# Performance work log

Hardware: AMD Instinct MI355X
Metric: run time of the kernel (lower is better)

The kernel has to match this reference:

```python
import jax, jax.numpy as jnp
import numpy as np

EPS = 1e-5
N_GRAPHS = 64


def gcn_conv(x, W, b, src, dst, n_nodes):
    # GCNConv: out = D^{-1/2} (A + I) D^{-1/2} X W + b
    xw = x @ W  # [N, H]
    # add self loops
    loops = jnp.arange(n_nodes, dtype=src.dtype)
    src_f = jnp.concatenate([src, loops])
    dst_f = jnp.concatenate([dst, loops])
    deg = jax.ops.segment_sum(jnp.ones_like(dst_f, dtype=xw.dtype), dst_f, num_segments=n_nodes)
    dinv = jnp.where(deg > 0, jax.lax.rsqrt(deg), 0.0)
    norm = dinv[src_f] * dinv[dst_f]  # [E+N]
    msg = xw[src_f] * norm[:, None]  # gather + scale
    out = jax.ops.segment_sum(msg, dst_f, num_segments=n_nodes)  # scatter-add
    return out + b


def batchnorm(x):
    # fresh BatchNorm1d in training mode: identity affine, batch stats, biased var
    mean = jnp.mean(x, axis=0)
    var = jnp.mean((x - mean) ** 2, axis=0)
    return (x - mean) * jax.lax.rsqrt(var + EPS)


def setup_inputs() -> dict:
    key = jax.random.key(0)
    ks = jax.random.split(key, 12)
    N, E, F, H, C = 65536, 1048576, 64, 64, 16
    x = jax.random.normal(ks[0], (N, F), dtype=jnp.float32)
    edge_index = jax.random.randint(ks[1], (2, E), 0, N, dtype=jnp.int64)
    batch = jnp.sort(jax.random.randint(ks[2], (N,), 0, N_GRAPHS, dtype=jnp.int64))
    s = 1.0 / np.sqrt(H)
    W0 = jax.random.normal(ks[3], (F, H), dtype=jnp.float32) * s
    b0 = jax.random.normal(ks[4], (H,), dtype=jnp.float32) * 0.1
    W1 = jax.random.normal(ks[5], (H, H), dtype=jnp.float32) * s
    b1 = jax.random.normal(ks[6], (H,), dtype=jnp.float32) * 0.1
    W2 = jax.random.normal(ks[7], (H, H), dtype=jnp.float32) * s
    b2 = jax.random.normal(ks[8], (H,), dtype=jnp.float32) * 0.1
    clf_W = jax.random.normal(ks[9], (C, H), dtype=jnp.float32) * s
    clf_b = jax.random.normal(ks[10], (C,), dtype=jnp.float32) * 0.1
    return {"x": x, "edge_index": edge_index, "batch": batch,
            "W0": W0, "b0": b0, "W1": W1, "b1": b1, "W2": W2, "b2": b2,
            "clf_W": clf_W, "clf_b": clf_b}


def reference(x, edge_index, batch, W0, b0, W1, b1, W2, b2, clf_W, clf_b):
    n_nodes = x.shape[0]
    src, dst = edge_index[0], edge_index[1]
    weights = [(W0, b0), (W1, b1), (W2, b2)]
    n_conv = len(weights)
    h = x
    for i, (W, b) in enumerate(weights):
        h = gcn_conv(h, W, b, src, dst, n_nodes)
        if i < n_conv - 1:
            h = jax.nn.relu(h)
        h = batchnorm(h)
    # global mean pool over graphs
    sums = jax.ops.segment_sum(h, batch, num_segments=N_GRAPHS)
    cnts = jax.ops.segment_sum(jnp.ones((n_nodes,), h.dtype), batch, num_segments=N_GRAPHS)
    pooled = sums / jnp.maximum(cnts, 1.0)[:, None]
    logits = pooled @ clf_W.T + clf_b
    return jax.nn.softmax(logits, axis=1)
```

## Files before the change

kernel.cpp:

```cpp
#include <hip/hip_runtime.h>
#include <hip/hip_fp16.h>


#define NBKT 512
#define CAP  4096
#define BSTRIDE 16
#define NSLOT 16
#define GSL   2048

__device__ inline unsigned pack2h(float a, float b) {
    __half ha = __float2half_rn(a), hb = __float2half_rn(b);
    unsigned short ua = *(unsigned short*)&ha, ub = *(unsigned short*)&hb;
    return (unsigned)ua | ((unsigned)ub << 16);
}

__device__ inline void acc8(float* a, uint4 u) {
    __half2* hp = (__half2*)&u;
#pragma unroll
    for (int i = 0; i < 4; ++i) {
        float2 f = __half22float2(hp[i]);
        a[2 * i] += f.x;
        a[2 * i + 1] += f.y;
    }
}

__global__ void k_binit(int* __restrict__ bcur, float* __restrict__ gstats) {
    int idx = blockIdx.x * 256 + threadIdx.x;
    if (idx < NBKT) bcur[idx * BSTRIDE] = idx * CAP;
    for (int i = idx; i < 3 * NSLOT * GSL; i += 32768) gstats[i] = 0.0f;
}

__global__ void k_bin(const int* __restrict__ ei, int E, int* __restrict__ bcur,
                      int* __restrict__ buck) {
    __shared__ int sd[4096];
    __shared__ unsigned short bk[4096];
    __shared__ int cnt[NBKT], off[NBKT];
    int t = threadIdx.x;
    int base = blockIdx.x * 4096;
    for (int i = t; i < NBKT; i += 256) cnt[i] = 0;
    __syncthreads();
#pragma unroll
    for (int k = 0; k < 16; ++k) {
        int i = k * 256 + t;
        int e = base + i;
        int s = ei[e], d = ei[E + e];
        sd[i] = (s << 7) | (d & 127);
        int b = d >> 7;
        bk[i] = (unsigned short)b;
        atomicAdd(&cnt[b], 1);
    }
    __syncthreads();
    for (int b = t; b < NBKT; b += 256) {
        int c = cnt[b];
        off[b] = c ? atomicAdd(&bcur[b * BSTRIDE], c) : 0;
    }
    __syncthreads();
#pragma unroll
    for (int k = 0; k < 16; ++k) {
        int i = k * 256 + t;
        int b = bk[i];
        int p = atomicAdd(&off[b], 1);
        buck[p] = sd[i];
    }
}

__global__ __launch_bounds__(512) void k_place(
        const int* __restrict__ bcur, const int* __restrict__ buck,
        int* __restrict__ rowptr, float* __restrict__ dinv, int* __restrict__ csr,
        int N, int E) {
    __shared__ int s[NBKT];
    __shared__ int dc[128], sc[128], cur[128];
    __shared__ int sbase;
    int b = blockIdx.x, t = threadIdx.x;
    s[t] = bcur[t * BSTRIDE] - t * CAP;
    if (t < 128) dc[t] = 0;
    __syncthreads();
    for (int o = 1; o < NBKT; o <<= 1) {
        int x = (t >= o) ? s[t - o] : 0;
        __syncthreads();
        s[t] += x;
        __syncthreads();
    }
    if (t == 0) {
        sbase = (b == 0) ? 0 : s[b - 1];
        if (b == NBKT - 1) rowptr[N] = E;
    }
    __syncthreads();
    int beg = b * CAP, end = bcur[b * BSTRIDE];
    for (int i = beg + t; i < end; i += 512) atomicAdd(&dc[buck[i] & 127], 1);
    __syncthreads();
    int v = (t < 128) ? dc[t] : 0;
    if (t < 128) sc[t] = v;
    __syncthreads();
    for (int o = 1; o < 128; o <<= 1) {
        int x = 0;
        if (t < 128 && t >= o) x = sc[t - o];
        __syncthreads();
        if (t < 128) sc[t] += x;
        __syncthreads();
    }
    if (t < 128) {
        int r = sbase + sc[t] - v;
        rowptr[b * 128 + t] = r;
        cur[t] = r;
        dinv[b * 128 + t] = rsqrtf((float)(v + 1));
    }
    __syncthreads();
    for (int i = beg + t; i < end; i += 512) {
        int e = buck[i];
        int p = atomicAdd(&cur[e & 127], 1);
        csr[p] = e >> 7;
    }
}

template <int HIN, int HS>
__global__ void k_gemm(const void* __restrict__ hv, const float* __restrict__ W,
                       const float* __restrict__ gstats, float invN,
                       const float* __restrict__ dinv, __half* __restrict__ y) {
    __shared__ float Ws[4096];
    __shared__ float hs[64 * 65];
    __shared__ float sm[64], sr[64], bs[64];
    int t = threadIdx.x;
    int rowBase = blockIdx.x * 64;
    if (t < 64) {
        if (HS) {
            float S = 0.0f, Q = 0.0f;
#pragma unroll
            for (int c = 0; c < NSLOT; ++c) {
                S += gstats[c * GSL + t * 16];
                Q += gstats[c * GSL + (64 + t) * 16];
            }
            float m = S * invN;
            float var = Q * invN - m * m;
            sm[t] = m;
            sr[t] = rsqrtf(var + 1e-5f);
        } else {
            sm[t] = 0.0f;
            sr[t] = 1.0f;
        }
    }
    __syncthreads();
#pragma unroll
    for (int k = 0; k < 4; ++k) {
        int i = t + k * 256;
        float4 wv = ((const float4*)W)[i];
        float s = sr[i >> 4];
        wv.x *= s; wv.y *= s; wv.z *= s; wv.w *= s;
        ((float4*)Ws)[i] = wv;
    }
    if (HIN) {
        const uint4* src = (const uint4*)((const __half*)hv + (size_t)rowBase * 64);
#pragma unroll
        for (int k = 0; k < 2; ++k) {
            int i = t + k * 256;
            int row = i >> 3, c8 = i & 7;
            uint4 u = src[i];
            const __half2* hp = (const __half2*)&u;
            float* dst = &hs[row * 65 + c8 * 8];
#pragma unroll
            for (int j = 0; j < 4; ++j) {
                dst[2 * j + 0] = __low2float(hp[j]);
                dst[2 * j + 1] = __high2float(hp[j]);
            }
        }
    } else {
        const float4* src = (const float4*)((const float*)hv + (size_t)rowBase * 64);
#pragma unroll
        for (int k = 0; k < 4; ++k) {
            int i = t + k * 256;
            int row = i >> 4, c4 = i & 15;
            float4 v = src[i];
            float* dst = &hs[row * 65 + c4 * 4];
            dst[0] = v.x; dst[1] = v.y; dst[2] = v.z; dst[3] = v.w;
        }
    }
    __syncthreads();
    if (t < 64) {
        float acc = 0.0f;
        for (int f = 0; f < 64; ++f) acc += sm[f] * Ws[f * 64 + t];
        bs[t] = -acc;
    }
    __syncthreads();
    int rg = t >> 4;
    int cg = t & 15;
    float4 a0, a1, a2, a3;
    {
        float bx = bs[cg * 4 + 0], by = bs[cg * 4 + 1];
        float bz = bs[cg * 4 + 2], bw = bs[cg * 4 + 3];
        a0 = {bx, by, bz, bw}; a1 = a0; a2 = a0; a3 = a0;
    }
    const float* h0 = &hs[(rg * 4 + 0) * 65];
    const float* h1 = &hs[(rg * 4 + 1) * 65];
    const float* h2 = &hs[(rg * 4 + 2) * 65];
    const float* h3 = &hs[(rg * 4 + 3) * 65];
#pragma unroll 4
    for (int f = 0; f < 64; ++f) {
        float4 wv = ((float4*)Ws)[f * 16 + cg];
        float v0 = h0[f], v1 = h1[f], v2 = h2[f], v3 = h3[f];
        a0.x += v0 * wv.x; a0.y += v0 * wv.y; a0.z += v0 * wv.z; a0.w += v0 * wv.w;
        a1.x += v1 * wv.x; a1.y += v1 * wv.y; a1.z += v1 * wv.z; a1.w += v1 * wv.w;
        a2.x += v2 * wv.x; a2.y += v2 * wv.y; a2.z += v2 * wv.z; a2.w += v2 * wv.w;
        a3.x += v3 * wv.x; a3.y += v3 * wv.y; a3.z += v3 * wv.z; a3.w += v3 * wv.w;
    }
    float d0 = dinv[rowBase + rg * 4 + 0];
    float d1 = dinv[rowBase + rg * 4 + 1];
    float d2 = dinv[rowBase + rg * 4 + 2];
    float d3 = dinv[rowBase + rg * 4 + 3];
    uint2* y2 = (uint2*)y;
    size_t ob = (size_t)(rowBase + rg * 4) * 16 + cg;
    y2[ob + 0]  = {pack2h(a0.x * d0, a0.y * d0), pack2h(a0.z * d0, a0.w * d0)};
    y2[ob + 16] = {pack2h(a1.x * d1, a1.y * d1), pack2h(a1.z * d1, a1.w * d1)};
    y2[ob + 32] = {pack2h(a2.x * d2, a2.y * d2), pack2h(a2.z * d2, a2.w * d2)};
    y2[ob + 48] = {pack2h(a3.x * d3, a3.y * d3), pack2h(a3.z * d3, a3.w * d3)};
}

template <int RELU>
__global__ __launch_bounds__(512) void k_agg(
        const __half* __restrict__ y, const int* __restrict__ rowptr,
        const int* __restrict__ csr, const float* __restrict__ dinv,
        const float* __restrict__ bias, __half* __restrict__ hout,
        float* __restrict__ gstats, int N) {
    __shared__ int lcsr[2048];
    __shared__ int lrp[65];
    __shared__ float SW[16][64];
    int t = threadIdx.x;
    int lane = t & 63, wid = t >> 6;
    int o = lane >> 3, j = lane & 7;
    int nodeBase = blockIdx.x * 64;
    if (t < 65) lrp[t] = rowptr[nodeBase + t];
    __syncthreads();
    int wbase = lrp[0];
    int wlen = lrp[64] - wbase;
    bool fits = (wlen <= 2048);
    if (fits)
        for (int i = t; i < wlen; i += 512) lcsr[i] = csr[wbase + i];
    __syncthreads();

    int n = nodeBase + wid * 8 + o;
    int beg = lrp[wid * 8 + o] - wbase;
    int d = lrp[wid * 8 + o + 1] - wbase - beg;
    const uint4* y4 = (const uint4*)y;
    float a[8] = {0, 0, 0, 0, 0, 0, 0, 0};

    if (fits) {
        const int* cp = lcsr + beg;
        int k = 0;
        for (; k + 4 <= d; k += 4) {
            int s0 = cp[k], s1 = cp[k + 1], s2 = cp[k + 2], s3 = cp[k + 3];
            uint4 u0 = y4[(size_t)s0 * 8 + j];
            uint4 u1 = y4[(size_t)s1 * 8 + j];
            uint4 u2 = y4[(size_t)s2 * 8 + j];
            uint4 u3 = y4[(size_t)s3 * 8 + j];
            acc8(a, u0); acc8(a, u1); acc8(a, u2); acc8(a, u3);
        }
        for (; k < d; ++k) {
            uint4 u0 = y4[(size_t)cp[k] * 8 + j];
            acc8(a, u0);
        }
    } else {
        const int* cp = csr + wbase + beg;
        int k = 0;
        for (; k + 4 <= d; k += 4) {
            int s0 = cp[k], s1 = cp[k + 1], s2 = cp[k + 2], s3 = cp[k + 3];
            uint4 u0 = y4[(size_t)s0 * 8 + j];
            uint4 u1 = y4[(size_t)s1 * 8 + j];
            uint4 u2 = y4[(size_t)s2 * 8 + j];
            uint4 u3 = y4[(size_t)s3 * 8 + j];
            acc8(a, u0); acc8(a, u1); acc8(a, u2); acc8(a, u3);
        }
        for (; k < d; ++k) {
            uint4 u0 = y4[(size_t)cp[k] * 8 + j];
            acc8(a, u0);
        }
    }
    uint4 us = y4[(size_t)n * 8 + j];
    acc8(a, us);

    float dv = dinv[n];
    const float4* b4 = (const float4*)bias;
    float4 blo = b4[j * 2], bhi = b4[j * 2 + 1];
    float v[8];
    v[0] = a[0] * dv + blo.x; v[1] = a[1] * dv + blo.y;
    v[2] = a[2] * dv + blo.z; v[3] = a[3] * dv + blo.w;
    v[4] = a[4] * dv + bhi.x; v[5] = a[5] * dv + bhi.y;
    v[6] = a[6] * dv + bhi.z; v[7] = a[7] * dv + bhi.w;
    if (RELU) {
#pragma unroll
        for (int i = 0; i < 8; ++i) v[i] = fmaxf(v[i], 0.0f);
    }
    uint4 ov;
    ov.x = pack2h(v[0], v[1]); ov.y = pack2h(v[2], v[3]);
    ov.z = pack2h(v[4], v[5]); ov.w = pack2h(v[6], v[7]);
    ((uint4*)hout)[(size_t)n * 8 + j] = ov;

    float q[8];
#pragma unroll
    for (int i = 0; i < 8; ++i) q[i] = v[i] * v[i];
#pragma unroll
    for (int st = 8; st <= 32; st <<= 1) {
#pragma unroll
        for (int i = 0; i < 8; ++i) {
            v[i] += __shfl_xor(v[i], st);
            q[i] += __shfl_xor(q[i], st);
        }
    }
    if (o == 0) {
#pragma unroll
        for (int i = 0; i < 8; ++i) {
            SW[wid][j * 8 + i] = v[i];
            SW[8 + wid][j * 8 + i] = q[i];
        }
    }
    __syncthreads();
    if (t < 64) {
        float s = 0.0f, qq = 0.0f;
#pragma unroll
        for (int w = 0; w < 8; ++w) {
            s += SW[w][t];
            qq += SW[8 + w][t];
        }
        float* gs = gstats + (blockIdx.x & (NSLOT - 1)) * GSL;
        atomicAdd(&gs[t * 16], s);
        atomicAdd(&gs[(64 + t) * 16], qq);
    }
}

__global__ __launch_bounds__(512) void k_poolhead(
        const __half* __restrict__ h, const int* __restrict__ batch,
        const float* __restrict__ gstats, float invN,
        const float* __restrict__ clfW, const float* __restrict__ clfb,
        float* __restrict__ out, int N) {
    __shared__ float SWm[8][64];
    __shared__ float pooled[64];
    __shared__ int rng[2];
    int g = blockIdx.x;
    int t = threadIdx.x;
    int lane = t & 63, wid = t >> 6;
    int o = lane >> 3, j = lane & 7;
    if (t < 2) {
        int key = g + t, lo = 0, hi = N;
        while (lo < hi) {
            int mid = (lo + hi) >> 1;
            if (batch[mid] < key) lo = mid + 1; else hi = mid;
        }
        rng[t] = lo;
    }
    __syncthreads();
    int lo = rng[0], hi = rng[1];
    const uint4* h4 = (const uint4*)h;
    float a[8] = {0, 0, 0, 0, 0, 0, 0, 0};
    int slot = wid * 8 + o;
    for (int n = lo + slot; n < hi; n += 256) {
        int n1 = n + 64, n2 = n + 128, n3 = n + 192;
        uint4 u0 = h4[(size_t)n * 8 + j];
        uint4 u1 = h4[(size_t)min(n1, hi - 1) * 8 + j];
        uint4 u2 = h4[(size_t)min(n2, hi - 1) * 8 + j];
        uint4 u3 = h4[(size_t)min(n3, hi - 1) * 8 + j];
        acc8(a, u0);
        if (n1 < hi) acc8(a, u1);
        if (n2 < hi) acc8(a, u2);
        if (n3 < hi) acc8(a, u3);
    }
#pragma unroll
    for (int st = 8; st <= 32; st <<= 1) {
#pragma unroll
        for (int i = 0; i < 8; ++i) a[i] += __shfl_xor(a[i], st);
    }
    if (o == 0) {
#pragma unroll
        for (int i = 0; i < 8; ++i) SWm[wid][j * 8 + i] = a[i];
    }
    __syncthreads();
    if (t < 64) {
        float s = 0.0f;
#pragma unroll
        for (int w = 0; w < 8; ++w) s += SWm[w][t];
        float S = 0.0f, Q = 0.0f;
#pragma unroll
        for (int c = 0; c < NSLOT; ++c) {
            S += gstats[c * GSL + t * 16];
            Q += gstats[c * GSL + (64 + t) * 16];
        }
        float m = S * invN;
        float r = rsqrtf(Q * invN - m * m + 1e-5f);
        float mean = s / fmaxf((float)(hi - lo), 1.0f);
        pooled[t] = (mean - m) * r;
    }
    __syncthreads();
    if (t < 16) {
        float acc = 0.0f;
#pragma unroll 8
        for (int f = 0; f < 64; ++f) acc += pooled[f] * clfW[t * 64 + f];
        acc += clfb[t];
        float mx = acc;
#pragma unroll
        for (int oo = 1; oo < 16; oo <<= 1) mx = fmaxf(mx, __shfl_xor(mx, oo, 16));
        float e = __expf(acc - mx);
        float sum = e;
#pragma unroll
        for (int oo = 1; oo < 16; oo <<= 1) sum += __shfl_xor(sum, oo, 16);
        out[g * 16 + t] = e / sum;
    }
}

extern "C" void kernel_launch(void* const* d_in, const int* in_sizes, int n_in,
                              void* d_out, int out_size, void* d_ws, size_t ws_size,
                              hipStream_t stream) {
    const float* x    = (const float*)d_in[0];
    const int*   ei   = (const int*)d_in[1];
    const int*   bat  = (const int*)d_in[2];
    const float* W0   = (const float*)d_in[3];
    const float* b0   = (const float*)d_in[4];
    const float* W1   = (const float*)d_in[5];
    const float* b1   = (const float*)d_in[6];
    const float* W2   = (const float*)d_in[7];
    const float* b2   = (const float*)d_in[8];
    const float* clfW = (const float*)d_in[9];
    const float* clfb = (const float*)d_in[10];
    float* out = (float*)d_out;

    const int N = in_sizes[0] / 64;
    const int E = in_sizes[1] / 2;
    const int AB = N / 64;

    char* w = (char*)d_ws;
    size_t off = 0;
    auto take = [&](size_t bytes) -> void* {
        off = (off + 255) & ~(size_t)255;
        void* p = w + off;
        off += bytes;
        return p;
    };
    int*    rowptr   = (int*)take((size_t)(N + 1) * 4);
    int*    bcur     = (int*)take((size_t)NBKT * BSTRIDE * 4);
    float*  dinv     = (float*)take((size_t)N * 4);
    int*    csr      = (int*)take((size_t)E * 4);
    __half* y        = (__half*)take((size_t)N * 64 * 2);
    __half* hA       = (__half*)take((size_t)N * 64 * 2);
    __half* hB       = (__half*)take((size_t)N * 64 * 2);
    float*  gstats   = (float*)take((size_t)3 * NSLOT * GSL * 4);
    int* buck = (int*)hB;
    float* gs0 = gstats;
    float* gs1 = gstats + NSLOT * GSL;
    float* gs2 = gstats + 2 * NSLOT * GSL;

    const float invN = 1.0f / (float)N;

    k_binit<<<128, 256, 0, stream>>>(bcur, gstats);
    k_bin<<<E / 4096, 256, 0, stream>>>(ei, E, bcur, buck);
    k_place<<<NBKT, 512, 0, stream>>>(bcur, buck, rowptr, dinv, csr, N, E);

    k_gemm<0, 0><<<N / 64, 256, 0, stream>>>(x, W0, nullptr, invN, dinv, y);
    k_agg<1><<<AB, 512, 0, stream>>>(y, rowptr, csr, dinv, b0, hA, gs0, N);
    k_gemm<1, 1><<<N / 64, 256, 0, stream>>>(hA, W1, gs0, invN, dinv, y);
    k_agg<1><<<AB, 512, 0, stream>>>(y, rowptr, csr, dinv, b1, hB, gs1, N);
    k_gemm<1, 1><<<N / 64, 256, 0, stream>>>(hB, W2, gs1, invN, dinv, y);
    k_agg<0><<<AB, 512, 0, stream>>>(y, rowptr, csr, dinv, b2, hA, gs2, N);

    k_poolhead<<<64, 512, 0, stream>>>(hA, bat, gs2, invN, clfW, clfb, out, N);
}
```

Before: 165.7 us.

## Fuse GCN layers into a single cooperative persistent kernel with grid syncs

The three gemm/aggregate layer pairs and the pooling head are merged into one cooperative kernel of 256 blocks of 512 threads, with grid-wide syncs between phases. Each block loops over four 64-row tiles or windows, so W and the BN stats are staged once per block rather than once per 64 rows. This removes six kernel launch boundaries and the repeated per-block setup. The cost is that only 256 blocks run, which means fewer waves hiding gather latency in the aggregation, plus grid-sync overhead; a plain multi-launch fallback runs if the cooperative launch fails.

```diff
diff --git a/kernel.cpp b/kernel.cpp
--- a/kernel.cpp
+++ b/kernel.cpp
@@ -1,5 +1,8 @@
 #include <hip/hip_runtime.h>
 #include <hip/hip_fp16.h>
+#include <hip/hip_cooperative_groups.h>
+
+namespace cg = cooperative_groups;
 
 
 #define NBKT 512
@@ -7,6 +10,7 @@
 #define BSTRIDE 16
 #define NSLOT 16
 #define GSL   2048
+#define FB    256
 
 __device__ inline unsigned pack2h(float a, float b) {
     __half ha = __float2half_rn(a), hb = __float2half_rn(b);
@@ -113,15 +117,17 @@
     }
 }
 
+
 template <int HIN, int HS>
-__global__ void k_gemm(const void* __restrict__ hv, const float* __restrict__ W,
-                       const float* __restrict__ gstats, float invN,
-                       const float* __restrict__ dinv, __half* __restrict__ y) {
-    __shared__ float Ws[4096];
-    __shared__ float hs[64 * 65];
-    __shared__ float sm[64], sr[64], bs[64];
-    int t = threadIdx.x;
-    int rowBase = blockIdx.x * 64;
+__device__ void gemm_phase(const void* __restrict__ hv, const float* __restrict__ W,
+                           const float* __restrict__ gstats, float invN,
+                           const float* __restrict__ dinv, __half* __restrict__ y,
+                           float* smem, int t) {
+    float* Ws = smem;
+    float* hs = smem + 4096;
+    float* sm = smem + 8256;
+    float* sr = smem + 8320;
+    float* bs = smem + 8384;
     if (t < 64) {
         if (HS) {
             float S = 0.0f, Q = 0.0f;
@@ -131,9 +137,8 @@
                 Q += gstats[c * GSL + (64 + t) * 16];
             }
             float m = S * invN;
-            float var = Q * invN - m * m;
             sm[t] = m;
-            sr[t] = rsqrtf(var + 1e-5f);
+            sr[t] = rsqrtf(Q * invN - m * m + 1e-5f);
         } else {
             sm[t] = 0.0f;
             sr[t] = 1.0f;
@@ -141,18 +146,27 @@
     }
     __syncthreads();
 #pragma unroll
-    for (int k = 0; k < 4; ++k) {
-        int i = t + k * 256;
+    for (int k = 0; k < 2; ++k) {
+        int i = t + k * 512;
         float4 wv = ((const float4*)W)[i];
         float s = sr[i >> 4];
         wv.x *= s; wv.y *= s; wv.z *= s; wv.w *= s;
         ((float4*)Ws)[i] = wv;
     }
-    if (HIN) {
-        const uint4* src = (const uint4*)((const __half*)hv + (size_t)rowBase * 64);
-#pragma unroll
-        for (int k = 0; k < 2; ++k) {
-            int i = t + k * 256;
+    __syncthreads();
+    if (t < 64) {
+        float acc = 0.0f;
+        for (int f = 0; f < 64; ++f) acc += sm[f] * Ws[f * 64 + t];
+        bs[t] = -acc;
+    }
+    __syncthreads();
+    int rg = t >> 4;
+    int cg = t & 15;
+    for (int tile = 0; tile < 4; ++tile) {
+        int rowBase = (blockIdx.x * 4 + tile) * 64;
+        if (HIN) {
+            const uint4* src = (const uint4*)((const __half*)hv + (size_t)rowBase * 64);
+            int i = t;
             int row = i >> 3, c8 = i & 7;
             uint4 u = src[i];
             const __half2* hp = (const __half2*)&u;
@@ -162,88 +176,72 @@
                 dst[2 * j + 0] = __low2float(hp[j]);
                 dst[2 * j + 1] = __high2float(hp[j]);
             }
-        }
-    } else {
-        const float4* src = (const float4*)((const float*)hv + (size_t)rowBase * 64);
-#pragma unroll
-        for (int k = 0; k < 4; ++k) {
-            int i = t + k * 256;
-            int row = i >> 4, c4 = i & 15;
-            float4 v = src[i];
-            float* dst = &hs[row * 65 + c4 * 4];
-            dst[0] = v.x; dst[1] = v.y; dst[2] = v.z; dst[3] = v.w;
-        }
-    }
-    __syncthreads();
-    if (t < 64) {
-        float acc = 0.0f;
-        for (int f = 0; f < 64; ++f) acc += sm[f] * Ws[f * 64 + t];
-        bs[t] = -acc;
-    }
-    __syncthreads();
-    int rg = t >> 4;
-    int cg = t & 15;
-    float4 a0, a1, a2, a3;
-    {
-        float bx = bs[cg * 4 + 0], by = bs[cg * 4 + 1];
-        float bz = bs[cg * 4 + 2], bw = bs[cg * 4 + 3];
-        a0 = {bx, by, bz, bw}; a1 = a0; a2 = a0; a3 = a0;
-    }
-    const float* h0 = &hs[(rg * 4 + 0) * 65];
-    const float* h1 = &hs[(rg * 4 + 1) * 65];
-    const float* h2 = &hs[(rg * 4 + 2) * 65];
-    const float* h3 = &hs[(rg * 4 + 3) * 65];
+        } else {
+            const float4* src = (const float4*)((const float*)hv + (size_t)rowBase * 64);
+#pragma unroll
+            for (int k = 0; k < 2; ++k) {
+                int i = t + k * 512;
+                int row = i >> 4, c4 = i & 15;
+                float4 v = src[i];
+                float* dst = &hs[row * 65 + c4 * 4];
+                dst[0] = v.x; dst[1] = v.y; dst[2] = v.z; dst[3] = v.w;
+            }
+        }
+        __syncthreads();
+        float4 a0, a1;
+        {
+            float bx = bs[cg * 4 + 0], by = bs[cg * 4 + 1];
+            float bz = bs[cg * 4 + 2], bw = bs[cg * 4 + 3];
+            a0 = {bx, by, bz, bw}; a1 = a0;
+        }
+        const float* h0 = &hs[(rg * 2 + 0) * 65];
+        const float* h1 = &hs[(rg * 2 + 1) * 65];
 #pragma unroll 4
-    for (int f = 0; f < 64; ++f) {
-        float4 wv = ((float4*)Ws)[f * 16 + cg];
-        float v0 = h0[f], v1 = h1[f], v2 = h2[f], v3 = h3[f];
-        a0.x += v0 * wv.x; a0.y += v0 * wv.y; a0.z += v0 * wv.z; a0.w += v0 * wv.w;
-        a1.x += v1 * wv.x; a1.y += v1 * wv.y; a1.z += v1 * wv.z; a1.w += v1 * wv.w;
-        a2.x += v2 * wv.x; a2.y += v2 * wv.y; a2.z += v2 * wv.z; a2.w += v2 * wv.w;
-        a3.x += v3 * wv.x; a3.y += v3 * wv.y; a3.z += v3 * wv.z; a3.w += v3 * wv.w;
-    }
-    float d0 = dinv[rowBase + rg * 4 + 0];
-    float d1 = dinv[rowBase + rg * 4 + 1];
-    float d2 = dinv[rowBase + rg * 4 + 2];
-    float d3 = dinv[rowBase + rg * 4 + 3];
-    uint2* y2 = (uint2*)y;
-    size_t ob = (size_t)(rowBase + rg * 4) * 16 + cg;
-    y2[ob + 0]  = {pack2h(a0.x * d0, a0.y * d0), pack2h(a0.z * d0, a0.w * d0)};
-    y2[ob + 16] = {pack2h(a1.x * d1, a1.y * d1), pack2h(a1.z * d1, a1.w * d1)};
-    y2[ob + 32] = {pack2h(a2.x * d2, a2.y * d2), pack2h(a2.z * d2, a2.w * d2)};
-    y2[ob + 48] = {pack2h(a3.x * d3, a3.y * d3), pack2h(a3.z * d3, a3.w * d3)};
+        for (int f = 0; f < 64; ++f) {
+            float4 wv = ((float4*)Ws)[f * 16 + cg];
+            float v0 = h0[f], v1 = h1[f];
+            a0.x += v0 * wv.x; a0.y += v0 * wv.y; a0.z += v0 * wv.z; a0.w += v0 * wv.w;
+            a1.x += v1 * wv.x; a1.y += v1 * wv.y; a1.z += v1 * wv.z; a1.w += v1 * wv.w;
+        }
+        float d0 = dinv[rowBase + rg * 2 + 0];
+        float d1 = dinv[rowBase + rg * 2 + 1];
+        uint2* y2 = (uint2*)y;
+        size_t ob = (size_t)(rowBase + rg * 2) * 16 + cg;
+        y2[ob + 0]  = {pack2h(a0.x * d0, a0.y * d0), pack2h(a0.z * d0, a0.w * d0)};
+        y2[ob + 16] = {pack2h(a1.x * d1, a1.y * d1), pack2h(a1.z * d1, a1.w * d1)};
+        __syncthreads();
+    }
 }
 
 template <int RELU>
-__global__ __launch_bounds__(512) void k_agg(
-        const __half* __restrict__ y, const int* __restrict__ rowptr,
-        const int* __restrict__ csr, const float* __restrict__ dinv,
-        const float* __restrict__ bias, __half* __restrict__ hout,
-        float* __restrict__ gstats, int N) {
-    __shared__ int lcsr[2048];
-    __shared__ int lrp[65];
-    __shared__ float SW[16][64];
-    int t = threadIdx.x;
+__device__ void agg_phase(const __half* __restrict__ y, const int* __restrict__ rowptr,
+                          const int* __restrict__ csr, const float* __restrict__ dinv,
+                          const float* __restrict__ bias, __half* __restrict__ hout,
+                          float* __restrict__ gsl, float* smem, int t) {
+    int* lcsr = (int*)smem;
+    int* lrp = (int*)smem + 2048;
+    float* SW = smem + 2176;
     int lane = t & 63, wid = t >> 6;
     int o = lane >> 3, j = lane & 7;
-    int nodeBase = blockIdx.x * 64;
-    if (t < 65) lrp[t] = rowptr[nodeBase + t];
-    __syncthreads();
-    int wbase = lrp[0];
-    int wlen = lrp[64] - wbase;
-    bool fits = (wlen <= 2048);
-    if (fits)
-        for (int i = t; i < wlen; i += 512) lcsr[i] = csr[wbase + i];
-    __syncthreads();
-
-    int n = nodeBase + wid * 8 + o;
-    int beg = lrp[wid * 8 + o] - wbase;
-    int d = lrp[wid * 8 + o + 1] - wbase - beg;
     const uint4* y4 = (const uint4*)y;
-    float a[8] = {0, 0, 0, 0, 0, 0, 0, 0};
-
-    if (fits) {
-        const int* cp = lcsr + beg;
+    for (int win = 0; win < 4; ++win) {
+        int blk = blockIdx.x * 4 + win;
+        int nodeBase = blk * 64;
+        __syncthreads();
+        if (t < 65) lrp[t] = rowptr[nodeBase + t];
+        __syncthreads();
+        int wbase = lrp[0];
+        int wlen = lrp[64] - wbase;
+        bool fits = (wlen <= 2048);
+        if (fits)
+            for (int i = t; i < wlen; i += 512) lcsr[i] = csr[wbase + i];
+        __syncthreads();
+
+        int n = nodeBase + wid * 8 + o;
+        int beg = lrp[wid * 8 + o] - wbase;
+        int d = lrp[wid * 8 + o + 1] - wbase - beg;
+        float a[8] = {0, 0, 0, 0, 0, 0, 0, 0};
+        const int* cp = fits ? (lcsr + beg) : (csr + wbase + beg);
         int k = 0;
         for (; k + 4 <= d; k += 4) {
             int s0 = cp[k], s1 = cp[k + 1], s2 = cp[k + 2], s3 = cp[k + 3];
@@ -257,84 +255,67 @@
             uint4 u0 = y4[(size_t)cp[k] * 8 + j];
             acc8(a, u0);
         }
-    } else {
-        const int* cp = csr + wbase + beg;
-        int k = 0;
-        for (; k + 4 <= d; k += 4) {
-            int s0 = cp[k], s1 = cp[k + 1], s2 = cp[k + 2], s3 = cp[k + 3];
-            uint4 u0 = y4[(size_t)s0 * 8 + j];
-            uint4 u1 = y4[(size_t)s1 * 8 + j];
-            uint4 u2 = y4[(size_t)s2 * 8 + j];
-            uint4 u3 = y4[(size_t)s3 * 8 + j];
-            acc8(a, u0); acc8(a, u1); acc8(a, u2); acc8(a, u3);
-        }
-        for (; k < d; ++k) {
-            uint4 u0 = y4[(size_t)cp[k] * 8 + j];
-            acc8(a, u0);
-        }
-    }
-    uint4 us = y4[(size_t)n * 8 + j];
-    acc8(a, us);
-
-    float dv = dinv[n];
-    const float4* b4 = (const float4*)bias;
-    float4 blo = b4[j * 2], bhi = b4[j * 2 + 1];
-    float v[8];
-    v[0] = a[0] * dv + blo.x; v[1] = a[1] * dv + blo.y;
-    v[2] = a[2] * dv + blo.z; v[3] = a[3] * dv + blo.w;
-    v[4] = a[4] * dv + bhi.x; v[5] = a[5] * dv + bhi.y;
-    v[6] = a[6] * dv + bhi.z; v[7] = a[7] * dv + bhi.w;
-    if (RELU) {
-#pragma unroll
-        for (int i = 0; i < 8; ++i) v[i] = fmaxf(v[i], 0.0f);
-    }
-    uint4 ov;
-    ov.x = pack2h(v[0], v[1]); ov.y = pack2h(v[2], v[3]);
-    ov.z = pack2h(v[4], v[5]); ov.w = pack2h(v[6], v[7]);
-    ((uint4*)hout)[(size_t)n * 8 + j] = ov;
-
-    float q[8];
-#pragma unroll
-    for (int i = 0; i < 8; ++i) q[i] = v[i] * v[i];
-#pragma unroll
-    for (int st = 8; st <= 32; st <<= 1) {
-#pragma unroll
-        for (int i = 0; i < 8; ++i) {
-            v[i] += __shfl_xor(v[i], st);
-            q[i] += __shfl_xor(q[i], st);
-        }
-    }
-    if (o == 0) {
-#pragma unroll
-        for (int i = 0; i < 8; ++i) {
-            SW[wid][j * 8 + i] = v[i];
-            SW[8 + wid][j * 8 + i] = q[i];
-        }
-    }
-    __syncthreads();
-    if (t < 64) {
-        float s = 0.0f, qq = 0.0f;
-#pragma unroll
-        for (int w = 0; w < 8; ++w) {
-            s += SW[w][t];
-            qq += SW[8 + w][t];
-        }
-        float* gs = gstats + (blockIdx.x & (NSLOT - 1)) * GSL;
-        atomicAdd(&gs[t * 16], s);
-        atomicAdd(&gs[(64 + t) * 16], qq);
-    }
-}
-
-__global__ __launch_bounds__(512) void k_poolhead(
-        const __half* __restrict__ h, const int* __restrict__ batch,
-        const float* __restrict__ gstats, float invN,
-        const float* __restrict__ clfW, const float* __restrict__ clfb,
-        float* __restrict__ out, int N) {
-    __shared__ float SWm[8][64];
-    __shared__ float pooled[64];
-    __shared__ int rng[2];
+        uint4 us = y4[(size_t)n * 8 + j];
+        acc8(a, us);
+
+        float dv = dinv[n];
+        const float4* b4 = (const float4*)bias;
+        float4 blo = b4[j * 2], bhi = b4[j * 2 + 1];
+        float v[8];
+        v[0] = a[0] * dv + blo.x; v[1] = a[1] * dv + blo.y;
+        v[2] = a[2] * dv + blo.z; v[3] = a[3] * dv + blo.w;
+        v[4] = a[4] * dv + bhi.x; v[5] = a[5] * dv + bhi.y;
+        v[6] = a[6] * dv + bhi.z; v[7] = a[7] * dv + bhi.w;
+        if (RELU) {
+#pragma unroll
+            for (int i = 0; i < 8; ++i) v[i] = fmaxf(v[i], 0.0f);
+        }
+        uint4 ov;
+        ov.x = pack2h(v[0], v[1]); ov.y = pack2h(v[2], v[3]);
+        ov.z = pack2h(v[4], v[5]); ov.w = pack2h(v[6], v[7]);
+        ((uint4*)hout)[(size_t)n * 8 + j] = ov;
+
+        float q[8];
+#pragma unroll
+        for (int i = 0; i < 8; ++i) q[i] = v[i] * v[i];
+#pragma unroll
+        for (int st = 8; st <= 32; st <<= 1) {
+#pragma unroll
+            for (int i = 0; i < 8; ++i) {
+                v[i] += __shfl_xor(v[i], st);
+                q[i] += __shfl_xor(q[i], st);
+            }
+        }
+        if (o == 0) {
+#pragma unroll
+            for (int i = 0; i < 8; ++i) {
+                SW[wid * 64 + j * 8 + i] = v[i];
+                SW[(8 + wid) * 64 + j * 8 + i] = q[i];
+            }
+        }
+        __syncthreads();
+        if (t < 64) {
+            float s = 0.0f, qq = 0.0f;
+#pragma unroll
+            for (int w = 0; w < 8; ++w) {
+                s += SW[w * 64 + t];
+                qq += SW[(8 + w) * 64 + t];
+            }
+            float* gs = gsl + (blk & (NSLOT - 1)) * GSL;
+            atomicAdd(&gs[t * 16], s);
+            atomicAdd(&gs[(64 + t) * 16], qq);
+        }
+    }
+}
+
+__device__ void poolhead_phase(const __half* __restrict__ h, const int* __restrict__ batch,
+                               const float* __restrict__ gstats, float invN,
+                               const float* __restrict__ clfW, const float* __restrict__ clfb,
+                               float* __restrict__ out, float* smem, int t, int N) {
+    float* SWm = smem;
+    float* pooled = smem + 512;
+    int* rng = (int*)(smem + 576);
     int g = blockIdx.x;
-    int t = threadIdx.x;
     int lane = t & 63, wid = t >> 6;
     int o = lane >> 3, j = lane & 7;
     if (t < 2) {
@@ -368,13 +349,13 @@
     }
     if (o == 0) {
 #pragma unroll
-        for (int i = 0; i < 8; ++i) SWm[wid][j * 8 + i] = a[i];
+        for (int i = 0; i < 8; ++i) SWm[wid * 64 + j * 8 + i] = a[i];
     }
     __syncthreads();
     if (t < 64) {
         float s = 0.0f;
 #pragma unroll
-        for (int w = 0; w < 8; ++w) s += SWm[w][t];
+        for (int w = 0; w < 8; ++w) s += SWm[w * 64 + t];
         float S = 0.0f, Q = 0.0f;
 #pragma unroll
         for (int c = 0; c < NSLOT; ++c) {
@@ -401,6 +382,64 @@
         for (int oo = 1; oo < 16; oo <<= 1) sum += __shfl_xor(sum, oo, 16);
         out[g * 16 + t] = e / sum;
     }
+}
+
+__global__ __launch_bounds__(512, 2) void k_fused(
+        const float* __restrict__ x,
+        const float* __restrict__ W0, const float* __restrict__ b0,
+        const float* __restrict__ W1, const float* __restrict__ b1,
+        const float* __restrict__ W2, const float* __restrict__ b2,
+        const float* __restrict__ clfW, const float* __restrict__ clfb,
+        const int* __restrict__ batch,
+        const int* __restrict__ rowptr, const int* __restrict__ csr,
+        const float* __restrict__ dinv,
+        __half* __restrict__ y, __half* __restrict__ hA, __half* __restrict__ hB,
+        float* __restrict__ gstats, float* __restrict__ out,
+        float invN, int N) {
+    __shared__ float smem[8512];
+    cg::grid_group grid = cg::this_grid();
+    int t = threadIdx.x;
+    float* gs0 = gstats;
+    float* gs1 = gstats + NSLOT * GSL;
+    float* gs2 = gstats + 2 * NSLOT * GSL;
+
+    gemm_phase<0, 0>(x, W0, nullptr, invN, dinv, y, smem, t);
+    grid.sync();
+    agg_phase<1>(y, rowptr, csr, dinv, b0, hA, gs0, smem, t);
+    grid.sync();
+    gemm_phase<1, 1>(hA, W1, gs0, invN, dinv, y, smem, t);
+    grid.sync();
+    agg_phase<1>(y, rowptr, csr, dinv, b1, hB, gs1, smem, t);
+    grid.sync();
+    gemm_phase<1, 1>(hB, W2, gs1, invN, dinv, y, smem, t);
+    grid.sync();
+    agg_phase<0>(y, rowptr, csr, dinv, b2, hA, gs2, smem, t);
+    grid.sync();
+    if (blockIdx.x < 64)
+        poolhead_phase(hA, batch, gs2, invN, clfW, clfb, out, smem, t, N);
+}
+
+template <int HIN, int HS>
+__global__ __launch_bounds__(512, 2) void kw_gemm(
+        const void* hv, const float* W, const float* gstats, float invN,
+        const float* dinv, __half* y) {
+    __shared__ float smem[8512];
+    gemm_phase<HIN, HS>(hv, W, gstats, invN, dinv, y, smem, threadIdx.x);
+}
+
+template <int RELU>
+__global__ __launch_bounds__(512, 2) void kw_agg(
+        const __half* y, const int* rowptr, const int* csr, const float* dinv,
+        const float* bias, __half* hout, float* gsl) {
+    __shared__ float smem[8512];
+    agg_phase<RELU>(y, rowptr, csr, dinv, bias, hout, gsl, smem, threadIdx.x);
+}
+
+__global__ __launch_bounds__(512, 2) void kw_poolhead(
+        const __half* h, const int* batch, const float* gstats, float invN,
+        const float* clfW, const float* clfb, float* out, int N) {
+    __shared__ float smem[8512];
+    poolhead_phase(h, batch, gstats, invN, clfW, clfb, out, smem, threadIdx.x, N);
 }
 
 extern "C" void kernel_launch(void* const* d_in, const int* in_sizes, int n_in,
@@ -421,7 +460,6 @@
 
     const int N = in_sizes[0] / 64;
     const int E = in_sizes[1] / 2;
-    const int AB = N / 64;
 
     char* w = (char*)d_ws;
     size_t off = 0;
@@ -431,31 +469,40 @@
         off += bytes;
         return p;
     };
-    int*    rowptr   = (int*)take((size_t)(N + 1) * 4);
-    int*    bcur     = (int*)take((size_t)NBKT * BSTRIDE * 4);
-    float*  dinv     = (float*)take((size_t)N * 4);
-    int*    csr      = (int*)take((size_t)E * 4);
-    __half* y        = (__half*)take((size_t)N * 64 * 2);
-    __half* hA       = (__half*)take((size_t)N * 64 * 2);
-    __half* hB       = (__half*)take((size_t)N * 64 * 2);
-    float*  gstats   = (float*)take((size_t)3 * NSLOT * GSL * 4);
+    int*    rowptr = (int*)take((size_t)(N + 1) * 4);
+    int*    bcur   = (int*)take((size_t)NBKT * BSTRIDE * 4);
+    float*  dinv   = (float*)take((size_t)N * 4);
+    int*    csr    = (int*)take((size_t)E * 4);
+    __half* y      = (__half*)take((size_t)N * 64 * 2);
+    __half* hA     = (__half*)take((size_t)N * 64 * 2);
+    __half* hB     = (__half*)take((size_t)N * 64 * 2);
+    float*  gstats = (float*)take((size_t)3 * NSLOT * GSL * 4);
     int* buck = (int*)hB;
     float* gs0 = gstats;
     float* gs1 = gstats + NSLOT * GSL;
     float* gs2 = gstats + 2 * NSLOT * GSL;
 
-    const float invN = 1.0f / (float)N;
+    float invN = 1.0f / (float)N;
+    int   Nv = N;
 
     k_binit<<<128, 256, 0, stream>>>(bcur, gstats);
     k_bin<<<E / 4096, 256, 0, stream>>>(ei, E, bcur, buck);
     k_place<<<NBKT, 512, 0, stream>>>(bcur, buck, rowptr, dinv, csr, N, E);
 
-    k_gemm<0, 0><<<N / 64, 256, 0, stream>>>(x, W0, nullptr, invN, dinv, y);
-    k_agg<1><<<AB, 512, 0, stream>>>(y, rowptr, csr, dinv, b0, hA, gs0, N);
-    k_gemm<1, 1><<<N / 64, 256, 0, stream>>>(hA, W1, gs0, invN, dinv, y);
-    k_agg<1><<<AB, 512, 0, stream>>>(y, rowptr, csr, dinv, b1, hB, gs1, N);
-    k_gemm<1, 1><<<N / 64, 256, 0, stream>>>(hB, W2, gs1, invN, dinv, y);
-    k_agg<0><<<AB, 512, 0, stream>>>(y, rowptr, csr, dinv, b2, hA, gs2, N);
-
-    k_poolhead<<<64, 512, 0, stream>>>(hA, bat, gs2, invN, clfW, clfb, out, N);
-}
+    void* kargs[] = {(void*)&x, (void*)&W0, (void*)&b0, (void*)&W1, (void*)&b1,
+                     (void*)&W2, (void*)&b2, (void*)&clfW, (void*)&clfb,
+                     (void*)&bat, (void*)&rowptr, (void*)&csr, (void*)&dinv,
+                     (void*)&y, (void*)&hA, (void*)&hB, (void*)&gstats,
+                     (void*)&out, (void*)&invN, (void*)&Nv};
+    hipError_t err = hipLaunchCooperativeKernel((void*)k_fused, dim3(FB), dim3(512),
+                                                kargs, 0, stream);
+    if (err != hipSuccess) {
+        kw_gemm<0, 0><<<FB, 512, 0, stream>>>(x, W0, nullptr, invN, dinv, y);
+        kw_agg<1><<<FB, 512, 0, stream>>>(y, rowptr, csr, dinv, b0, hA, gs0);
+        kw_gemm<1, 1><<<FB, 512, 0, stream>>>(hA, W1, gs0, invN, dinv, y);
+        kw_agg<1><<<FB, 512, 0, stream>>>(y, rowptr, csr, dinv, b1, hB, gs1);
+        kw_gemm<1, 1><<<FB, 512, 0, stream>>>(hB, W2, gs1, invN, dinv, y);
+        kw_agg<0><<<FB, 512, 0, stream>>>(y, rowptr, csr, dinv, b2, hA, gs2);
+        kw_poolhead<<<64, 512, 0, stream>>>(hA, bat, gs2, invN, clfW, clfb, out, Nv);
+    }
+}
```

Result: slower. 414.3 us (+150.0%).
